# Optimization experiments

Hardware: AMD Instinct MI355X
Metric: run time of the kernel (lower is better)

Reference implementation:

```python
import jax, jax.numpy as jnp
import numpy as np

K = 3
CHUNK = 1000  # query chunk size for KNN distance tiles
EPS = 1e-8
GRID = 256.0  # coordinate extent (coords / stride in the original)


def _knn3(queries, refs):
    """Brute-force KNN (K=3, squared L2) computed in chunks to bound memory.
    queries: [Q,3], refs: [M,3] -> (dist [Q,3], idx [Q,3] int32)."""
    ref_sq = jnp.sum(refs * refs, axis=-1)  # [M]

    def chunk_fn(q):  # q: [CHUNK,3]
        d = jnp.sum(q * q, -1)[:, None] - 2.0 * (q @ refs.T) + ref_sq[None, :]
        d = jnp.maximum(d, 0.0)  # guard tiny negatives from cancellation
        neg_d, idx = jax.lax.top_k(-d, K)
        return -neg_d, idx

    Q = queries.shape[0]
    qs = queries.reshape(Q // CHUNK, CHUNK, 3)
    dists, idxs = jax.lax.map(chunk_fn, qs)
    return dists.reshape(Q, K), idxs.reshape(Q, K)


def setup_inputs() -> dict:
    key = jax.random.key(0)
    k1, k2, k3, k4 = jax.random.split(key, 4)
    N1, N2, C = 20000, 20000, 8
    xyz1 = jax.random.uniform(k1, (N1, 3), dtype=jnp.float32) * GRID
    point1 = jax.random.normal(k2, (N1, C), dtype=jnp.float32)
    xyz2 = jax.random.uniform(k3, (N2, 3), dtype=jnp.float32) * GRID
    motion = jax.random.normal(k4, (N2, C, 3), dtype=jnp.float32)
    return {"xyz1": xyz1, "point1": point1, "xyz2": xyz2, "motion": motion}


def reference(xyz1, point1, xyz2, motion):
    # Motion-compensated inter prediction tail of inter_prediction.forward:
    # per-channel warp, KNN(K=3) into frame 1, inverse-distance interpolation.
    N2, C, _ = motion.shape
    # xyz2_ = xyz2.unsqueeze(2) + motion -> [N2*C, 3]
    xyz2_ = (xyz2[:, None, :] + motion).reshape(N2 * C, 3)
    dist, idx = _knn3(xyz2_, xyz1)                 # [N2*C,3]
    dist = dist + EPS
    dist = dist.reshape(N2, C, K)
    idx = idx.reshape(N2, C, K)
    weights = 1.0 / dist
    weights = weights / jnp.maximum(weights.sum(axis=2, keepdims=True), 3.0)
    # knn_point1[n,c,k] = point1[idx[n,c,k], c]  (per-channel gather)
    pt = point1.T                                   # [C, N1]
    knn_point1 = pt[jnp.arange(C)[None, :, None], idx]  # [N2,C,3]
    predicted_point2 = (weights * knn_point1).sum(axis=2)  # [N2,C]
    return predicted_point2
```

## Files before the change

kernel.cpp:

```cpp
#include <hip/hip_runtime.h>
#include <math.h>

#define KNN_EPS 1e-8f
#define GH 16.0f
#define GC 16
#define NCELLS (GC * GC * GC)
#define MARGIN 1.0f
#define CAPR 64
#define CAPQ 192


__device__ __forceinline__ int cell_coord(float v) {
    int c = (int)floorf(v * (1.0f / GH));
    return min(max(c, 0), GC - 1);
}

__global__ void fused_scatter_kernel(
    const float* __restrict__ xyz1, int n1,
    const float* __restrict__ xyz2,
    const float* __restrict__ motion, int n2, int C,
    int* __restrict__ counts, int* __restrict__ qcounts,
    float4* __restrict__ rbuck, float4* __restrict__ qbuck,
    float4* __restrict__ refspill, int* __restrict__ rsn,
    float4* __restrict__ qspill, int* __restrict__ qsn)
{
#pragma clang fp contract(off)
    int i = blockIdx.x * blockDim.x + threadIdx.x;
    if (i < n1) {
        float x = xyz1[3 * i + 0];
        float y = xyz1[3 * i + 1];
        float z = xyz1[3 * i + 2];
        int cid = (cell_coord(z) * GC + cell_coord(y)) * GC + cell_coord(x);
        int pos = atomicAdd(&counts[cid], 1);
        float4 v = make_float4(x, y, z, __int_as_float(i));
        if (pos < CAPR) rbuck[cid * CAPR + pos] = v;
        else { int sp = atomicAdd(rsn, 1); refspill[sp] = v; }
    }
    int nq = n2 * C;
    if (i < nq) {
        int n = i / C;
        float qx = xyz2[3 * n + 0] + motion[3 * i + 0];
        float qy = xyz2[3 * n + 1] + motion[3 * i + 1];
        float qz = xyz2[3 * n + 2] + motion[3 * i + 2];
        int cid = (cell_coord(qz) * GC + cell_coord(qy)) * GC + cell_coord(qx);
        int pos = atomicAdd(&qcounts[cid], 1);
        float4 v = make_float4(qx, qy, qz, __int_as_float(i));
        if (pos < CAPQ) qbuck[cid * CAPQ + pos] = v;
        else { int sp = atomicAdd(qsn, 1); qspill[sp] = v; }
    }
}

__device__ __forceinline__ void top3_insert_lex(float d, int j,
                                                float& bd0, float& bd1, float& bd2,
                                                int& bi0, int& bi1, int& bi2) {
    if (d < bd2 || (d == bd2 && j < bi2)) {
        if (d < bd1 || (d == bd1 && j < bi1)) {
            bd2 = bd1; bi2 = bi1;
            if (d < bd0 || (d == bd0 && j < bi0)) {
                bd1 = bd0; bi1 = bi0;
                bd0 = d;   bi0 = j;
            } else {
                bd1 = d;   bi1 = j;
            }
        } else {
            bd2 = d;       bi2 = j;
        }
    }
}

__device__ __forceinline__ void eval_candidate(
    float4 r, float qx, float qy, float qz, float qsq,
    float& bd0, float& bd1, float& bd2, int& bi0, int& bi1, int& bi2) {
    int ridx = __float_as_int(r.w);
    float rsq = r.x * r.x + r.y * r.y;
    rsq = rsq + r.z * r.z;
    float t = fmaf(qz, r.z, fmaf(qy, r.y, qx * r.x));
    float h = qsq + rsq;
    float d = fmaxf(fmaf(-2.0f, t, h), 0.0f);
    top3_insert_lex(d, ridx, bd0, bd1, bd2, bi0, bi1, bi2);
}

__device__ __forceinline__ float cert_radius(float qx, float qy, float qz,
                                             int icx, int icy, int icz, int rho) {
    float R = INFINITY;
    if (icx - rho > 0)      R = fminf(R, qx - (float)(icx - rho) * GH);
    if (icx + rho < GC - 1) R = fminf(R, (float)(icx + rho + 1) * GH - qx);
    if (icy - rho > 0)      R = fminf(R, qy - (float)(icy - rho) * GH);
    if (icy + rho < GC - 1) R = fminf(R, (float)(icy + rho + 1) * GH - qy);
    if (icz - rho > 0)      R = fminf(R, qz - (float)(icz - rho) * GH);
    if (icz + rho < GC - 1) R = fminf(R, (float)(icz + rho + 1) * GH - qz);
    return R;
}

__device__ __forceinline__ void epilogue_store(
    float bd0, float bd1, float bd2, int bi0, int bi1, int bi2,
    int qid, int C, const float* __restrict__ point1, float* __restrict__ out) {
#pragma clang fp contract(off)
    float dd0 = bd0 + KNN_EPS;
    float dd1 = bd1 + KNN_EPS;
    float dd2 = bd2 + KNN_EPS;
    float w0 = 1.0f / dd0;
    float w1 = 1.0f / dd1;
    float w2 = 1.0f / dd2;
    float s  = w0 + w1;
    s = s + w2;
    float m = fmaxf(s, 3.0f);
    w0 = w0 / m;
    w1 = w1 / m;
    w2 = w2 / m;
    const int c = qid - (qid / C) * C;
    float p0 = point1[bi0 * C + c];
    float p1 = point1[bi1 * C + c];
    float p2 = point1[bi2 * C + c];
    float acc = w0 * p0 + w1 * p1;
    acc = acc + w2 * p2;
    out[qid] = acc;
}

__device__ void ring_search(float qx, float qy, float qz, float qsq,
                            const float4* __restrict__ rbuck,
                            const int* __restrict__ counts, int rspn,
                            const float4* __restrict__ refspill,
                            float& bd0, float& bd1, float& bd2,
                            int& bi0, int& bi1, int& bi2) {
    const int icx = cell_coord(qx);
    const int icy = cell_coord(qy);
    const int icz = cell_coord(qz);
    for (int k = 0; k < rspn; ++k)
        eval_candidate(refspill[k], qx, qy, qz, qsq, bd0, bd1, bd2, bi0, bi1, bi2);
    for (int rho = 0; rho < GC; ++rho) {
        for (int dz = -rho; dz <= rho; ++dz) {
            int cz = icz + dz;
            if (cz < 0 || cz >= GC) continue;
            int adz = (dz < 0) ? -dz : dz;
            for (int dy = -rho; dy <= rho; ++dy) {
                int cy = icy + dy;
                if (cy < 0 || cy >= GC) continue;
                int ady = (dy < 0) ? -dy : dy;
                int step = (adz == rho || ady == rho || rho == 0) ? 1 : 2 * rho;
                for (int dx = -rho; dx <= rho; dx += step) {
                    int cx = icx + dx;
                    if (cx < 0 || cx >= GC) continue;
                    int cid = (cz * GC + cy) * GC + cx;
                    int e = min(counts[cid], CAPR);
                    for (int s = 0; s < e; ++s)
                        eval_candidate(rbuck[cid * CAPR + s], qx, qy, qz, qsq,
                                       bd0, bd1, bd2, bi0, bi1, bi2);
                }
            }
        }
        float Rr = cert_radius(qx, qy, qz, icx, icy, icz, rho);
        if (bd2 + MARGIN <= Rr * Rr) break;
    }
}

__global__ __launch_bounds__(128, 8) void knn_cell_kernel(
    const float4* __restrict__ rbuck,
    const int*   __restrict__ counts,
    const float4* __restrict__ refspill,
    const int*   __restrict__ rsn,
    const float4* __restrict__ qbuck,
    const int*   __restrict__ qcounts,
    const float* __restrict__ point1,
    float* __restrict__ out,
    int C)
{
#pragma clang fp contract(off)
    const int cell = blockIdx.x;
    const int qn = min(qcounts[cell], CAPQ);
    if (qn == 0) return;
    const int qbase = cell * CAPQ;

    const int tid = threadIdx.x;
    const int lane = tid & 63;
    const int wave = tid >> 6;

    const int icx = cell & (GC - 1);
    const int icy = (cell >> 4) & (GC - 1);
    const int icz = cell >> 8;
    const int rspn = *rsn;

    for (int base = wave * 64; base < qn; base += 128) {
        const int qo = base + lane;
        const bool active = qo < qn;
        float4 Q = qbuck[qbase + (active ? qo : base)];
        const float qx = Q.x, qy = Q.y, qz = Q.z;
        const int qid = __float_as_int(Q.w);
        float qsq = qx * qx + qy * qy;
        qsq = qsq + qz * qz;

        float bd0 = INFINITY, bd1 = INFINITY, bd2 = INFINITY;
        int   bi0 = 0,        bi1 = 0,        bi2 = 0;

        for (int r = 0; r < 27; ++r) {
            const int dz = r / 9 - 1, dy = (r / 3) % 3 - 1, dx = r % 3 - 1;
            const int cz = icz + dz, cy = icy + dy, cx = icx + dx;
            if (cz < 0 || cz >= GC || cy < 0 || cy >= GC || cx < 0 || cx >= GC)
                continue;
            const int cid = (cz * GC + cy) * GC + cx;
            const int e = min(counts[cid], CAPR);
            const float4* __restrict__ cp = rbuck + (size_t)cid * CAPR;
            int s = 0;
            for (; s + 4 <= e; s += 4) {
                float4 c0 = cp[s + 0];
                float4 c1 = cp[s + 1];
                float4 c2 = cp[s + 2];
                float4 c3 = cp[s + 3];
                eval_candidate(c0, qx, qy, qz, qsq, bd0, bd1, bd2, bi0, bi1, bi2);
                eval_candidate(c1, qx, qy, qz, qsq, bd0, bd1, bd2, bi0, bi1, bi2);
                eval_candidate(c2, qx, qy, qz, qsq, bd0, bd1, bd2, bi0, bi1, bi2);
                eval_candidate(c3, qx, qy, qz, qsq, bd0, bd1, bd2, bi0, bi1, bi2);
            }
            for (; s < e; ++s)
                eval_candidate(cp[s], qx, qy, qz, qsq,
                               bd0, bd1, bd2, bi0, bi1, bi2);
        }

        for (int k = 0; k < rspn; ++k)
            eval_candidate(refspill[k], qx, qy, qz, qsq,
                           bd0, bd1, bd2, bi0, bi1, bi2);

        float R = cert_radius(qx, qy, qz, icx, icy, icz, 1);
        if (!(bd2 + MARGIN <= R * R)) {
            for (int rho = 2; rho < GC; ++rho) {
                for (int dz = -rho; dz <= rho; ++dz) {
                    int cz = icz + dz;
                    if (cz < 0 || cz >= GC) continue;
                    int adz = (dz < 0) ? -dz : dz;
                    for (int dy = -rho; dy <= rho; ++dy) {
                        int cy = icy + dy;
                        if (cy < 0 || cy >= GC) continue;
                        int ady = (dy < 0) ? -dy : dy;
                        int step = (adz == rho || ady == rho) ? 1 : 2 * rho;
                        for (int dx = -rho; dx <= rho; dx += step) {
                            int cx = icx + dx;
                            if (cx < 0 || cx >= GC) continue;
                            int cid = (cz * GC + cy) * GC + cx;
                            int e = min(counts[cid], CAPR);
                            for (int s = 0; s < e; ++s)
                                eval_candidate(rbuck[cid * CAPR + s],
                                               qx, qy, qz, qsq,
                                               bd0, bd1, bd2, bi0, bi1, bi2);
                        }
                    }
                }
                float Rr = cert_radius(qx, qy, qz, icx, icy, icz, rho);
                if (bd2 + MARGIN <= Rr * Rr) break;
            }
        }

        if (active)
            epilogue_store(bd0, bd1, bd2, bi0, bi1, bi2, qid, C, point1, out);
    }
}

__global__ __launch_bounds__(256) void qspill_kernel(
    const float4* __restrict__ qspill, const int* __restrict__ qsn,
    const float4* __restrict__ rbuck, const int* __restrict__ counts,
    const float4* __restrict__ refspill, const int* __restrict__ rsn,
    const float* __restrict__ point1, float* __restrict__ out, int C)
{
#pragma clang fp contract(off)
    const int nsp = *qsn;
    const int rspn = *rsn;
    for (int s = blockIdx.x * blockDim.x + threadIdx.x; s < nsp;
         s += gridDim.x * blockDim.x) {
        float4 Q = qspill[s];
        const float qx = Q.x, qy = Q.y, qz = Q.z;
        const int qid = __float_as_int(Q.w);
        float qsq = qx * qx + qy * qy;
        qsq = qsq + qz * qz;
        float bd0 = INFINITY, bd1 = INFINITY, bd2 = INFINITY;
        int   bi0 = 0,        bi1 = 0,        bi2 = 0;
        ring_search(qx, qy, qz, qsq, rbuck, counts, rspn, refspill,
                    bd0, bd1, bd2, bi0, bi1, bi2);
        epilogue_store(bd0, bd1, bd2, bi0, bi1, bi2, qid, C, point1, out);
    }
}

extern "C" void kernel_launch(void* const* d_in, const int* in_sizes, int n_in,
                              void* d_out, int out_size, void* d_ws, size_t ws_size,
                              hipStream_t stream) {
    const float* xyz1   = (const float*)d_in[0];
    const float* point1 = (const float*)d_in[1];
    const float* xyz2   = (const float*)d_in[2];
    const float* motion = (const float*)d_in[3];
    float* out = (float*)d_out;

    const int n1 = in_sizes[0] / 3;
    const int n2 = in_sizes[2] / 3;
    const int C  = in_sizes[1] / n1;
    const int nq = n2 * C;

    char* ws = (char*)d_ws;
    size_t off = 0;
    auto alloc = [&](size_t bytes) {
        char* p = ws + off;
        off = (off + bytes + 255) & ~(size_t)255;
        return p;
    };
    float4* rbuck    = (float4*)alloc((size_t)NCELLS * CAPR * 16);
    float4* qbuck    = (float4*)alloc((size_t)NCELLS * CAPQ * 16);
    float4* refspill = (float4*)alloc((size_t)n1 * 16);
    float4* qspill   = (float4*)alloc((size_t)nq * 16);
    int*    zero     = (int*)alloc((size_t)(2 * NCELLS + 2) * 4);
    int* counts  = zero;
    int* qcounts = zero + NCELLS;
    int* rsn     = zero + 2 * NCELLS;
    int* qsn     = zero + 2 * NCELLS + 1;

    const int nmax = (n1 > nq) ? n1 : nq;

    hipMemsetAsync(zero, 0, (size_t)(2 * NCELLS + 2) * 4, stream);
    fused_scatter_kernel<<<(nmax + 255) / 256, 256, 0, stream>>>(
        xyz1, n1, xyz2, motion, n2, C,
        counts, qcounts, rbuck, qbuck, refspill, rsn, qspill, qsn);
    knn_cell_kernel<<<NCELLS, 128, 0, stream>>>(
        rbuck, counts, refspill, rsn, qbuck, qcounts, point1, out, C);
    qspill_kernel<<<4, 256, 0, stream>>>(
        qspill, qsn, rbuck, counts, refspill, rsn, point1, out, C);
}
```

Measured before the change: 171.4 us.

## Stage 27-cell neighbor candidates in LDS and use single-wave blocks

Each block now loads up to 16 reference points from each of the 27 neighboring cells into shared memory once, then every query in the cell reads candidates from LDS instead of global memory. Any cell holding more than 16 points falls back to reading the remainder from global memory. Blocks shrink to one 64-thread wave that loops over all queries in the cell, which changes occupancy and per-block parallelism. The aim is to cut repeated global or L2 loads of the same neighbor points, at the cost of extra syncs and fewer threads per block.

```diff
diff --git a/kernel.cpp b/kernel.cpp
--- a/kernel.cpp
+++ b/kernel.cpp
@@ -8,6 +8,7 @@
 #define MARGIN 1.0f
 #define CAPR 64
 #define CAPQ 192
+#define SCAP 16
 
 
 __device__ __forceinline__ int cell_coord(float v) {
@@ -154,7 +155,7 @@
     }
 }
 
-__global__ __launch_bounds__(128, 8) void knn_cell_kernel(
+__global__ __launch_bounds__(64, 4) void knn_cell_kernel(
     const float4* __restrict__ rbuck,
     const int*   __restrict__ counts,
     const float4* __restrict__ refspill,
@@ -170,17 +171,37 @@
     const int qn = min(qcounts[cell], CAPQ);
     if (qn == 0) return;
     const int qbase = cell * CAPQ;
-
-    const int tid = threadIdx.x;
-    const int lane = tid & 63;
-    const int wave = tid >> 6;
+    const int lane = threadIdx.x;
 
     const int icx = cell & (GC - 1);
     const int icy = (cell >> 4) & (GC - 1);
     const int icz = cell >> 8;
     const int rspn = *rsn;
 
-    for (int base = wave * 64; base < qn; base += 128) {
+    __shared__ float4 cand[27 * SCAP];
+    __shared__ int lds_cid[27];
+    __shared__ int lds_len[27];
+
+    if (lane < 27) {
+        int dz = lane / 9 - 1, dy = (lane / 3) % 3 - 1, dx = lane % 3 - 1;
+        int cz = icz + dz, cy = icy + dy, cx = icx + dx;
+        int ok = (cz >= 0 && cz < GC && cy >= 0 && cy < GC && cx >= 0 && cx < GC);
+        int cid = ok ? (cz * GC + cy) * GC + cx : 0;
+        lds_cid[lane] = cid;
+        lds_len[lane] = ok ? min(counts[cid], CAPR) : 0;
+    }
+    __syncthreads();
+
+    for (int j = lane; j < 27 * SCAP; j += 64) {
+        int r = j >> 4;
+        int s = j & (SCAP - 1);
+        int len = lds_len[r];
+        if (s < min(len, SCAP))
+            cand[j] = rbuck[lds_cid[r] * CAPR + s];
+    }
+    __syncthreads();
+
+    for (int base = 0; base < qn; base += 64) {
         const int qo = base + lane;
         const bool active = qo < qn;
         float4 Q = qbuck[qbase + (active ? qo : base)];
@@ -193,27 +214,29 @@
         int   bi0 = 0,        bi1 = 0,        bi2 = 0;
 
         for (int r = 0; r < 27; ++r) {
-            const int dz = r / 9 - 1, dy = (r / 3) % 3 - 1, dx = r % 3 - 1;
-            const int cz = icz + dz, cy = icy + dy, cx = icx + dx;
-            if (cz < 0 || cz >= GC || cy < 0 || cy >= GC || cx < 0 || cx >= GC)
-                continue;
-            const int cid = (cz * GC + cy) * GC + cx;
-            const int e = min(counts[cid], CAPR);
-            const float4* __restrict__ cp = rbuck + (size_t)cid * CAPR;
+            const int len = __builtin_amdgcn_readfirstlane(lds_len[r]);
+            const int e = min(len, SCAP);
+            const int cb = r << 4;
             int s = 0;
             for (; s + 4 <= e; s += 4) {
-                float4 c0 = cp[s + 0];
-                float4 c1 = cp[s + 1];
-                float4 c2 = cp[s + 2];
-                float4 c3 = cp[s + 3];
+                float4 c0 = cand[cb + s + 0];
+                float4 c1 = cand[cb + s + 1];
+                float4 c2 = cand[cb + s + 2];
+                float4 c3 = cand[cb + s + 3];
                 eval_candidate(c0, qx, qy, qz, qsq, bd0, bd1, bd2, bi0, bi1, bi2);
                 eval_candidate(c1, qx, qy, qz, qsq, bd0, bd1, bd2, bi0, bi1, bi2);
                 eval_candidate(c2, qx, qy, qz, qsq, bd0, bd1, bd2, bi0, bi1, bi2);
                 eval_candidate(c3, qx, qy, qz, qsq, bd0, bd1, bd2, bi0, bi1, bi2);
             }
             for (; s < e; ++s)
-                eval_candidate(cp[s], qx, qy, qz, qsq,
+                eval_candidate(cand[cb + s], qx, qy, qz, qsq,
                                bd0, bd1, bd2, bi0, bi1, bi2);
+            if (len > SCAP) {
+                const int cid = __builtin_amdgcn_readfirstlane(lds_cid[r]);
+                for (int t = SCAP; t < len; ++t)
+                    eval_candidate(rbuck[cid * CAPR + t], qx, qy, qz, qsq,
+                                   bd0, bd1, bd2, bi0, bi1, bi2);
+            }
         }
 
         for (int k = 0; k < rspn; ++k)
@@ -315,7 +338,7 @@
     fused_scatter_kernel<<<(nmax + 255) / 256, 256, 0, stream>>>(
         xyz1, n1, xyz2, motion, n2, C,
         counts, qcounts, rbuck, qbuck, refspill, rsn, qspill, qsn);
-    knn_cell_kernel<<<NCELLS, 128, 0, stream>>>(
+    knn_cell_kernel<<<NCELLS, 64, 0, stream>>>(
         rbuck, counts, refspill, rsn, qbuck, qcounts, point1, out, C);
     qspill_kernel<<<4, 256, 0, stream>>>(
         qspill, qsn, rbuck, counts, refspill, rsn, point1, out, C);
```

After: 184.5 us. +7.6%, slower.

## Drop query bucketing; split 27-cell neighbourhood across four waves per query group

Applied to the files above, without the earlier changes.

Removes the query scatter into per-cell buckets and the query spill kernel, so each query is now computed directly from xyz2+motion in query order. Each block handles 64 queries with four waves, and each wave scans up to 7 of the 27 neighbouring cells. Partial top-3 lists are merged through shared memory, and wave 0 runs any extended ring search and the epilogue. CAPR shrinks to 16 to cut bucket footprint. The cost is more reference spill to scan (about 5 refs per cell on average, so overflow is frequent), uncoalesced query locality, and a block-wide sync.

```diff
diff --git a/kernel.cpp b/kernel.cpp
--- a/kernel.cpp
+++ b/kernel.cpp
@@ -6,8 +6,7 @@
 #define GC 16
 #define NCELLS (GC * GC * GC)
 #define MARGIN 1.0f
-#define CAPR 64
-#define CAPQ 192
+#define CAPR 16
 
 
 __device__ __forceinline__ int cell_coord(float v) {
@@ -15,39 +14,23 @@
     return min(max(c, 0), GC - 1);
 }
 
-__global__ void fused_scatter_kernel(
+__global__ void scatter_ref_kernel(
     const float* __restrict__ xyz1, int n1,
-    const float* __restrict__ xyz2,
-    const float* __restrict__ motion, int n2, int C,
-    int* __restrict__ counts, int* __restrict__ qcounts,
-    float4* __restrict__ rbuck, float4* __restrict__ qbuck,
-    float4* __restrict__ refspill, int* __restrict__ rsn,
-    float4* __restrict__ qspill, int* __restrict__ qsn)
+    int* __restrict__ counts,
+    float4* __restrict__ rbuck,
+    float4* __restrict__ refspill, int* __restrict__ rsn)
 {
 #pragma clang fp contract(off)
     int i = blockIdx.x * blockDim.x + threadIdx.x;
-    if (i < n1) {
-        float x = xyz1[3 * i + 0];
-        float y = xyz1[3 * i + 1];
-        float z = xyz1[3 * i + 2];
-        int cid = (cell_coord(z) * GC + cell_coord(y)) * GC + cell_coord(x);
-        int pos = atomicAdd(&counts[cid], 1);
-        float4 v = make_float4(x, y, z, __int_as_float(i));
-        if (pos < CAPR) rbuck[cid * CAPR + pos] = v;
-        else { int sp = atomicAdd(rsn, 1); refspill[sp] = v; }
-    }
-    int nq = n2 * C;
-    if (i < nq) {
-        int n = i / C;
-        float qx = xyz2[3 * n + 0] + motion[3 * i + 0];
-        float qy = xyz2[3 * n + 1] + motion[3 * i + 1];
-        float qz = xyz2[3 * n + 2] + motion[3 * i + 2];
-        int cid = (cell_coord(qz) * GC + cell_coord(qy)) * GC + cell_coord(qx);
-        int pos = atomicAdd(&qcounts[cid], 1);
-        float4 v = make_float4(qx, qy, qz, __int_as_float(i));
-        if (pos < CAPQ) qbuck[cid * CAPQ + pos] = v;
-        else { int sp = atomicAdd(qsn, 1); qspill[sp] = v; }
-    }
+    if (i >= n1) return;
+    float x = xyz1[3 * i + 0];
+    float y = xyz1[3 * i + 1];
+    float z = xyz1[3 * i + 2];
+    int cid = (cell_coord(z) * GC + cell_coord(y)) * GC + cell_coord(x);
+    int pos = atomicAdd(&counts[cid], 1);
+    float4 v = make_float4(x, y, z, __int_as_float(i));
+    if (pos < CAPR) rbuck[cid * CAPR + pos] = v;
+    else { int sp = atomicAdd(rsn, 1); refspill[sp] = v; }
 }
 
 __device__ __forceinline__ void top3_insert_lex(float d, int j,
@@ -117,108 +100,97 @@
     out[qid] = acc;
 }
 
-__device__ void ring_search(float qx, float qy, float qz, float qsq,
-                            const float4* __restrict__ rbuck,
-                            const int* __restrict__ counts, int rspn,
-                            const float4* __restrict__ refspill,
-                            float& bd0, float& bd1, float& bd2,
-                            int& bi0, int& bi1, int& bi2) {
-    const int icx = cell_coord(qx);
-    const int icy = cell_coord(qy);
-    const int icz = cell_coord(qz);
-    for (int k = 0; k < rspn; ++k)
-        eval_candidate(refspill[k], qx, qy, qz, qsq, bd0, bd1, bd2, bi0, bi1, bi2);
-    for (int rho = 0; rho < GC; ++rho) {
-        for (int dz = -rho; dz <= rho; ++dz) {
-            int cz = icz + dz;
-            if (cz < 0 || cz >= GC) continue;
-            int adz = (dz < 0) ? -dz : dz;
-            for (int dy = -rho; dy <= rho; ++dy) {
-                int cy = icy + dy;
-                if (cy < 0 || cy >= GC) continue;
-                int ady = (dy < 0) ? -dy : dy;
-                int step = (adz == rho || ady == rho || rho == 0) ? 1 : 2 * rho;
-                for (int dx = -rho; dx <= rho; dx += step) {
-                    int cx = icx + dx;
-                    if (cx < 0 || cx >= GC) continue;
-                    int cid = (cz * GC + cy) * GC + cx;
-                    int e = min(counts[cid], CAPR);
-                    for (int s = 0; s < e; ++s)
-                        eval_candidate(rbuck[cid * CAPR + s], qx, qy, qz, qsq,
-                                       bd0, bd1, bd2, bi0, bi1, bi2);
-                }
-            }
-        }
-        float Rr = cert_radius(qx, qy, qz, icx, icy, icz, rho);
-        if (bd2 + MARGIN <= Rr * Rr) break;
-    }
-}
-
-__global__ __launch_bounds__(128, 8) void knn_cell_kernel(
+__global__ __launch_bounds__(256, 4) void knn_query_kernel(
+    const float* __restrict__ xyz2,
+    const float* __restrict__ motion,
     const float4* __restrict__ rbuck,
     const int*   __restrict__ counts,
     const float4* __restrict__ refspill,
     const int*   __restrict__ rsn,
-    const float4* __restrict__ qbuck,
-    const int*   __restrict__ qcounts,
     const float* __restrict__ point1,
     float* __restrict__ out,
-    int C)
+    int nq, int C)
 {
 #pragma clang fp contract(off)
-    const int cell = blockIdx.x;
-    const int qn = min(qcounts[cell], CAPQ);
-    if (qn == 0) return;
-    const int qbase = cell * CAPQ;
-
-    const int tid = threadIdx.x;
+    const int tid  = threadIdx.x;
     const int lane = tid & 63;
-    const int wave = tid >> 6;
-
-    const int icx = cell & (GC - 1);
-    const int icy = (cell >> 4) & (GC - 1);
-    const int icz = cell >> 8;
-    const int rspn = *rsn;
-
-    for (int base = wave * 64; base < qn; base += 128) {
-        const int qo = base + lane;
-        const bool active = qo < qn;
-        float4 Q = qbuck[qbase + (active ? qo : base)];
-        const float qx = Q.x, qy = Q.y, qz = Q.z;
-        const int qid = __float_as_int(Q.w);
-        float qsq = qx * qx + qy * qy;
-        qsq = qsq + qz * qz;
-
-        float bd0 = INFINITY, bd1 = INFINITY, bd2 = INFINITY;
-        int   bi0 = 0,        bi1 = 0,        bi2 = 0;
-
-        for (int r = 0; r < 27; ++r) {
+    const int slab = tid >> 6;
+    const int qi   = blockIdx.x * 64 + lane;
+    const bool active = qi < nq;
+    const int i = active ? qi : 0;
+    const int n = i / C;
+
+    const float qx = xyz2[3 * n + 0] + motion[3 * i + 0];
+    const float qy = xyz2[3 * n + 1] + motion[3 * i + 1];
+    const float qz = xyz2[3 * n + 2] + motion[3 * i + 2];
+    float qsq = qx * qx + qy * qy;
+    qsq = qsq + qz * qz;
+
+    const int icx = cell_coord(qx);
+    const int icy = cell_coord(qy);
+    const int icz = cell_coord(qz);
+
+    float bd0 = INFINITY, bd1 = INFINITY, bd2 = INFINITY;
+    int   bi0 = 0,        bi1 = 0,        bi2 = 0;
+
+    int es[7];
+#pragma unroll
+    for (int rr = 0; rr < 7; ++rr) {
+        const int r = slab * 7 + rr;
+        int e = 0;
+        if (r < 27) {
             const int dz = r / 9 - 1, dy = (r / 3) % 3 - 1, dx = r % 3 - 1;
             const int cz = icz + dz, cy = icy + dy, cx = icx + dx;
-            if (cz < 0 || cz >= GC || cy < 0 || cy >= GC || cx < 0 || cx >= GC)
-                continue;
-            const int cid = (cz * GC + cy) * GC + cx;
-            const int e = min(counts[cid], CAPR);
-            const float4* __restrict__ cp = rbuck + (size_t)cid * CAPR;
-            int s = 0;
-            for (; s + 4 <= e; s += 4) {
-                float4 c0 = cp[s + 0];
-                float4 c1 = cp[s + 1];
-                float4 c2 = cp[s + 2];
-                float4 c3 = cp[s + 3];
-                eval_candidate(c0, qx, qy, qz, qsq, bd0, bd1, bd2, bi0, bi1, bi2);
-                eval_candidate(c1, qx, qy, qz, qsq, bd0, bd1, bd2, bi0, bi1, bi2);
-                eval_candidate(c2, qx, qy, qz, qsq, bd0, bd1, bd2, bi0, bi1, bi2);
-                eval_candidate(c3, qx, qy, qz, qsq, bd0, bd1, bd2, bi0, bi1, bi2);
-            }
-            for (; s < e; ++s)
-                eval_candidate(cp[s], qx, qy, qz, qsq,
-                               bd0, bd1, bd2, bi0, bi1, bi2);
-        }
-
+            if ((unsigned)cz < GC && (unsigned)cy < GC && (unsigned)cx < GC) {
+                const int cid = (cz * GC + cy) * GC + cx;
+                e = min(counts[cid], CAPR);
+            }
+        }
+        es[rr] = e;
+    }
+
+#pragma unroll
+    for (int rr = 0; rr < 7; ++rr) {
+        const int r = slab * 7 + rr;
+        if (r < 27) {
+            const int e = es[rr];
+            if (e > 0) {
+                const int dz = r / 9 - 1, dy = (r / 3) % 3 - 1, dx = r % 3 - 1;
+                const int cid = ((icz + dz) * GC + (icy + dy)) * GC + (icx + dx);
+                const float4* __restrict__ cp = rbuck + cid * CAPR;
+                for (int s = 0; s < e; ++s)
+                    eval_candidate(cp[s], qx, qy, qz, qsq,
+                                   bd0, bd1, bd2, bi0, bi1, bi2);
+            }
+        }
+    }
+
+    if (slab == 3) {
+        const int rspn = *rsn;
         for (int k = 0; k < rspn; ++k)
             eval_candidate(refspill[k], qx, qy, qz, qsq,
                            bd0, bd1, bd2, bi0, bi1, bi2);
+    }
+
+    __shared__ float pbd[3][64][3];
+    __shared__ int   pbi[3][64][3];
+    if (slab > 0) {
+        pbd[slab - 1][lane][0] = bd0; pbi[slab - 1][lane][0] = bi0;
+        pbd[slab - 1][lane][1] = bd1; pbi[slab - 1][lane][1] = bi1;
+        pbd[slab - 1][lane][2] = bd2; pbi[slab - 1][lane][2] = bi2;
+    }
+    __syncthreads();
+
+    if (slab == 0) {
+#pragma unroll
+        for (int sl = 0; sl < 3; ++sl)
+#pragma unroll
+            for (int m = 0; m < 3; ++m) {
+                float d = pbd[sl][lane][m];
+                if (d < INFINITY)
+                    top3_insert_lex(d, pbi[sl][lane][m],
+                                    bd0, bd1, bd2, bi0, bi1, bi2);
+            }
 
         float R = cert_radius(qx, qy, qz, icx, icy, icz, 1);
         if (!(bd2 + MARGIN <= R * R)) {
@@ -250,31 +222,7 @@
         }
 
         if (active)
-            epilogue_store(bd0, bd1, bd2, bi0, bi1, bi2, qid, C, point1, out);
-    }
-}
-
-__global__ __launch_bounds__(256) void qspill_kernel(
-    const float4* __restrict__ qspill, const int* __restrict__ qsn,
-    const float4* __restrict__ rbuck, const int* __restrict__ counts,
-    const float4* __restrict__ refspill, const int* __restrict__ rsn,
-    const float* __restrict__ point1, float* __restrict__ out, int C)
-{
-#pragma clang fp contract(off)
-    const int nsp = *qsn;
-    const int rspn = *rsn;
-    for (int s = blockIdx.x * blockDim.x + threadIdx.x; s < nsp;
-         s += gridDim.x * blockDim.x) {
-        float4 Q = qspill[s];
-        const float qx = Q.x, qy = Q.y, qz = Q.z;
-        const int qid = __float_as_int(Q.w);
-        float qsq = qx * qx + qy * qy;
-        qsq = qsq + qz * qz;
-        float bd0 = INFINITY, bd1 = INFINITY, bd2 = INFINITY;
-        int   bi0 = 0,        bi1 = 0,        bi2 = 0;
-        ring_search(qx, qy, qz, qsq, rbuck, counts, rspn, refspill,
-                    bd0, bd1, bd2, bi0, bi1, bi2);
-        epilogue_store(bd0, bd1, bd2, bi0, bi1, bi2, qid, C, point1, out);
+            epilogue_store(bd0, bd1, bd2, bi0, bi1, bi2, qi, C, point1, out);
     }
 }
 
@@ -300,23 +248,14 @@
         return p;
     };
     float4* rbuck    = (float4*)alloc((size_t)NCELLS * CAPR * 16);
-    float4* qbuck    = (float4*)alloc((size_t)NCELLS * CAPQ * 16);
     float4* refspill = (float4*)alloc((size_t)n1 * 16);
-    float4* qspill   = (float4*)alloc((size_t)nq * 16);
-    int*    zero     = (int*)alloc((size_t)(2 * NCELLS + 2) * 4);
-    int* counts  = zero;
-    int* qcounts = zero + NCELLS;
-    int* rsn     = zero + 2 * NCELLS;
-    int* qsn     = zero + 2 * NCELLS + 1;
-
-    const int nmax = (n1 > nq) ? n1 : nq;
-
-    hipMemsetAsync(zero, 0, (size_t)(2 * NCELLS + 2) * 4, stream);
-    fused_scatter_kernel<<<(nmax + 255) / 256, 256, 0, stream>>>(
-        xyz1, n1, xyz2, motion, n2, C,
-        counts, qcounts, rbuck, qbuck, refspill, rsn, qspill, qsn);
-    knn_cell_kernel<<<NCELLS, 128, 0, stream>>>(
-        rbuck, counts, refspill, rsn, qbuck, qcounts, point1, out, C);
-    qspill_kernel<<<4, 256, 0, stream>>>(
-        qspill, qsn, rbuck, counts, refspill, rsn, point1, out, C);
-}
+    int*    zero     = (int*)alloc((size_t)(NCELLS + 1) * 4);
+    int* counts = zero;
+    int* rsn    = zero + NCELLS;
+
+    hipMemsetAsync(zero, 0, (size_t)(NCELLS + 1) * 4, stream);
+    scatter_ref_kernel<<<(n1 + 255) / 256, 256, 0, stream>>>(
+        xyz1, n1, counts, rbuck, refspill, rsn);
+    knn_query_kernel<<<(nq + 63) / 64, 256, 0, stream>>>(
+        xyz2, motion, rbuck, counts, refspill, rsn, point1, out, nq, C);
+}
```

Measured after the change: 215.3 us. +25.6%, slower.
